# Kernel optimization log

Measured on AMD Instinct MI355X. Metric: run time of the kernel, lower is better.

The kernel has to match this reference:

```python
import jax, jax.numpy as jnp
import numpy as np

B, H, CI, O = 8, 16, 16, 16          # batch, child spatial, child caps, parent caps
K, S, ROUTINGS = 3, 1, 3             # kernel, stride, EM iterations
FINAL_LAMBDA = 0.01
EPS = 1e-9


def setup_inputs() -> dict:
    key = jax.random.key(0)
    k1, k2, k3, k4, k5 = jax.random.split(key, 5)
    inputs_pose = jax.random.normal(k1, (B, H, H, CI, 16), dtype=jnp.float32)
    inputs_activation = jax.random.uniform(k2, (B, H, H, CI, 1), dtype=jnp.float32)
    # transformation matrices: [1, k*k*child_caps, parent_caps, 4, 4]
    w = jax.random.normal(k3, (1, K * K * CI, O, 4, 4), dtype=jnp.float32)
    beta_a = jax.random.normal(k4, (O,), dtype=jnp.float32)
    beta_v = jax.random.normal(k5, (O,), dtype=jnp.float32)
    return {"inputs_pose": inputs_pose, "inputs_activation": inputs_activation,
            "w": w, "beta_a": beta_a, "beta_v": beta_v}


def _extract_patches(x, k, s):
    # kernel_tile: im2col-like gather. x: [B, H, W, ...] -> [B, p, p, k, k, ...]
    Hs = x.shape[1]
    p = (Hs - k) // s + 1
    idx = (jnp.arange(p) * s)[:, None] + jnp.arange(k)[None, :]      # [p, k]
    xh = x[:, idx]                   # [B, ph, kh, W, ...]
    patches = xh[:, :, :, idx]       # [B, ph, kh, pw, kw, ...]
    return jnp.swapaxes(patches, 2, 3), p


def _child_index_map(Hs, k, s, p):
    # flat child spatial index feeding each (parent pos, kernel slot)
    ph = np.arange(p)[:, None] * s + np.arange(k)[None, :]           # [p, k]
    ch = ph[:, None, :, None] * Hs + ph[None, :, None, :]            # [p, p, k, k]
    return ch.reshape(p * p, k * k)                                   # [P2, K2]


def reference(inputs_pose, inputs_activation, w, beta_a, beta_v):
    P = (H - K) // S + 1
    P2, K2 = P * P, K * K
    K2CI = K2 * CI

    # ---- kernel_tile ----
    pose_t, _ = _extract_patches(inputs_pose, K, S)       # [B,P,P,K,K,CI,16]
    act_t, _ = _extract_patches(inputs_activation, K, S)  # [B,P,P,K,K,CI,1]
    pose_unroll = pose_t.reshape(B * P2, K2CI, 4, 4)
    act_unroll = act_t.reshape(B * P2, K2CI)

    # ---- compute_votes: tiny 4x4 matmuls per (child slot, parent cap) ----
    votes = jnp.einsum('nkpq,koqr->nkopr', pose_unroll, w[0])  # [B*P2,K2CI,O,4,4]
    votes = votes.reshape(B, P2, K2CI, O, 16)
    act_i = act_unroll.reshape(B, P2, K2CI, 1, 1)

    # ---- spatial routing bookkeeping (static integers) ----
    child_idx = _child_index_map(H, K, S, P)                    # [P2, K2]
    kk_child = np.repeat(child_idx, CI, axis=1)                 # [P2, K2CI]
    counts = np.zeros(H * H, np.float32)
    np.add.at(counts, child_idx.reshape(-1), 1.0)               # parents per child pos
    cap_id = np.tile(np.arange(CI), K2)                         # [K2CI]
    seg = jnp.asarray((kk_child * CI + cap_id[None, :]).reshape(-1))  # [P2*K2CI]
    n_seg = H * H * CI

    # initial routing: uniform over all (parent pos, parent cap) each child feeds
    rr0 = 1.0 / (O * counts[kk_child])                          # [P2, K2CI]
    rr = jnp.asarray(rr0)[None, :, :, None, None]               # bcast [1,P2,K2CI,1,1]

    beta_a_b = beta_a.reshape(1, 1, 1, O, 1)
    beta_v_b = beta_v.reshape(1, 1, 1, O, 1)

    mean = act_j = None
    for it in range(ROUTINGS):
        inv_temp = FINAL_LAMBDA * (1.0 - 0.95 ** (it + 1))
        # ---- M-step: weighted Gaussian statistics ----
        rr_prime = rr * act_i                                   # [B,P2,K2CI,O,1]
        rr_sum = jnp.sum(rr_prime, axis=2, keepdims=True) + EPS # [B,P2,1,O,1]
        mean = jnp.sum(rr_prime * votes, axis=2, keepdims=True) / rr_sum
        var = jnp.sum(rr_prime * jnp.square(votes - mean), axis=2, keepdims=True) / rr_sum + EPS
        cost_h = (beta_v_b + 0.5 * jnp.log(var)) * rr_sum       # [B,P2,1,O,16]
        cost = jnp.sum(cost_h, axis=-1, keepdims=True)          # [B,P2,1,O,1]
        act_j = jax.nn.sigmoid(inv_temp * (beta_a_b - cost))    # [B,P2,1,O,1]
        # ---- E-step: softmax over all (parent pos, parent cap) per child capsule ----
        if it < ROUTINGS - 1:
            log_p = -0.5 * jnp.sum(jnp.square(votes - mean) / var
                                   + jnp.log(2.0 * np.pi * var), axis=-1)  # [B,P2,K2CI,O]
            zz = jnp.log(act_j[..., 0] + EPS) + log_p           # [B,P2,K2CI,O]
            z = jnp.transpose(zz, (1, 2, 0, 3)).reshape(P2 * K2CI, B, O)
            row_max = jnp.max(z, axis=-1)                       # [P2*K2CI, B]
            seg_max = jax.ops.segment_max(row_max, seg, num_segments=n_seg)
            g = seg_max[seg][..., None]
            ez = jnp.exp(z - g)
            denom = jax.ops.segment_sum(jnp.sum(ez, axis=-1), seg, num_segments=n_seg)[seg]
            rr_new = ez / (denom[..., None] + EPS)              # sums to 1 per child capsule
            rr = jnp.transpose(rr_new.reshape(P2, K2CI, B, O), (2, 0, 1, 3))[..., None]

    pose_out = mean[:, :, 0].reshape(B, P, P, O, 16)
    act_out = act_j[:, :, 0].reshape(B, P, P, O, 1)
    return pose_out, act_out
```

## Files before the change

### kernel.cpp

```cpp
#include <hip/hip_runtime.h>

namespace {
constexpr int B_ = 8, H_ = 16, CI_ = 16, O_ = 16, P_ = 14;
constexpr int P2_ = P_ * P_;
constexpr int K2CI_ = 144;
constexpr int NV_ = 2304;
constexpr float EPS_ = 1e-9f;
constexpr float LOG2PI_ = 1.8378770664093453f;

using f2 = __attribute__((ext_vector_type(2))) float;

__device__ __forceinline__ float cnt1(int h) {
  int lo = (h - (P_ - 1)) > 0 ? (h - (P_ - 1)) : 0;
  int hi = h < 2 ? h : 2;
  return (float)(hi - lo + 1);
}

__global__ __launch_bounds__(256) void transpose_all(const float* __restrict__ pose,
                                                     float* __restrict__ pose_t,
                                                     const float* __restrict__ w,
                                                     float* __restrict__ wt) {
  if (blockIdx.x < 2048) {
    const int i = blockIdx.x * 256 + threadIdx.x;
    const int cell = i >> 4, idx = i & 15;
    const int p = idx >> 2, q = idx & 3;
    pose_t[(cell << 4) + (q << 2) + p] = pose[i];
  } else {
    const int i = (blockIdx.x - 2048) * 256 + threadIdx.x;
    const int ko = i >> 4, q = (i >> 2) & 3, r = i & 3;
    wt[(ko << 4) + (r << 2) + q] = w[i];
  }
}

template <int MODE>
__global__ __launch_bounds__(512, 8) void caps_main(
    const float* __restrict__ pose_t, const float* __restrict__ act,
    const float* __restrict__ wt, const float* __restrict__ beta_a,
    const float* __restrict__ beta_v, const float* __restrict__ zin,
    const float* __restrict__ gmax, const float* __restrict__ gden,
    float* __restrict__ zout, float* __restrict__ out) {
  __shared__ float rr_s[(MODE == 0) ? K2CI_ : NV_];
  __shared__ f2 partv[4][512];
  __shared__ float partr[512];
  __shared__ f2 sfin[4][64];
  __shared__ float sfr[64];
  __shared__ float gm_s[(MODE == 0) ? 1 : K2CI_];
  __shared__ float ad_s[(MODE == 0) ? 1 : K2CI_];

  const int tid = threadIdx.x;
  const int wv = __builtin_amdgcn_readfirstlane(tid >> 6);
  const int l = tid & 63;
  const int o = l >> 2, r = l & 3;
  const int pid = blockIdx.x;
  const int b = pid / P2_;
  const int p2 = pid - b * P2_;
  const int pi = p2 / P_;
  const int pj = p2 - pi * P_;
  const float inv_temp = (MODE == 0) ? 0.0005f : (MODE == 1) ? 0.000975f : 0.00142625f;

  if (MODE == 0) {
    if (tid < K2CI_) {
      const int ci = tid & 15, kk = tid >> 4;
      const int ki = (kk >= 6) ? 2 : (kk >= 3) ? 1 : 0, kj = kk - 3 * ki;
      const int cidx = ((b * H_ + pi + ki) * H_ + pj + kj) * CI_ + ci;
      rr_s[tid] = act[cidx] / (16.0f * cnt1(pi + ki) * cnt1(pj + kj));
    }
  } else {
    if (tid < K2CI_) {
      const int ci = tid & 15, kk = tid >> 4;
      const int ki = (kk >= 6) ? 2 : (kk >= 3) ? 1 : 0, kj = kk - 3 * ki;
      const int cidx = ((b * H_ + pi + ki) * H_ + pj + kj) * CI_ + ci;
      gm_s[tid] = gmax[cidx];
      ad_s[tid] = act[cidx] / (gden[cidx] + EPS_);
    }
    __syncthreads();
    for (int i4 = tid; i4 < NV_ / 4; i4 += 512) {
      const float4 z4 = ((const float4*)(zin + (size_t)pid * NV_))[i4];
      const int k = i4 >> 2;
      const float gmk = gm_s[k], adk = ad_s[k];
      float4 r4;
      r4.x = __expf(z4.x - gmk) * adk;
      r4.y = __expf(z4.y - gmk) * adk;
      r4.z = __expf(z4.z - gmk) * adk;
      r4.w = __expf(z4.w - gmk) * adk;
      ((float4*)rr_s)[i4] = r4;
    }
  }
  __syncthreads();

  const float bvo = 16.0f * beta_v[o];
  const float bao = beta_a[o];

  const float* pose_b = pose_t + ((size_t)((b * H_ + pi) * H_ + pj) << 8);
  const float* wt_l = wt + (l << 2);
  const int ci0 = wv * 2;

#define WT_OFF(idx) ((((idx) >> 1) << 12) + ((ci0 + ((idx)&1)) << 8))
#define PB_OFF(idx) (((((idx) >> 1) / 3) << 12) + ((((idx) >> 1) % 3) << 8) + ((ci0 + ((idx)&1)) << 4))

  float prr = 0.f;
  f2 pm01 = {0.f, 0.f}, pm23 = {0.f, 0.f}, pv01 = {0.f, 0.f}, pv23 = {0.f, 0.f};
  {
    float4 wbuf0 = *(const float4*)(wt_l + WT_OFF(0));
    float4 wbuf1 = *(const float4*)(wt_l + WT_OFF(1));
#pragma unroll
    for (int idx = 0; idx < 18; ++idx) {
      const float4 w4 = (idx & 1) ? wbuf1 : wbuf0;
      if (idx < 16) {
        if (idx & 1)
          wbuf1 = *(const float4*)(wt_l + WT_OFF(idx + 2));
        else
          wbuf0 = *(const float4*)(wt_l + WT_OFF(idx + 2));
      }
      const float* pb = pose_b + PB_OFF(idx);
      const float4 P0 = *(const float4*)(pb);
      const float4 P1 = *(const float4*)(pb + 4);
      const float4 P2 = *(const float4*)(pb + 8);
      const float4 P3 = *(const float4*)(pb + 12);
      f2 v01 = (f2){P0.x, P0.y} * w4.x;
      f2 v23 = (f2){P0.z, P0.w} * w4.x;
      v01 = __builtin_elementwise_fma((f2){P1.x, P1.y}, (f2){w4.y, w4.y}, v01);
      v23 = __builtin_elementwise_fma((f2){P1.z, P1.w}, (f2){w4.y, w4.y}, v23);
      v01 = __builtin_elementwise_fma((f2){P2.x, P2.y}, (f2){w4.z, w4.z}, v01);
      v23 = __builtin_elementwise_fma((f2){P2.z, P2.w}, (f2){w4.z, w4.z}, v23);
      v01 = __builtin_elementwise_fma((f2){P3.x, P3.y}, (f2){w4.w, w4.w}, v01);
      v23 = __builtin_elementwise_fma((f2){P3.z, P3.w}, (f2){w4.w, w4.w}, v23);
      const int k = ((idx >> 1) << 4) + ci0 + (idx & 1);
      const float rrk = (MODE == 0) ? rr_s[k] : rr_s[(k << 4) + o];
      prr += rrk;
      const f2 rr2 = {rrk, rrk};
      const f2 a01 = rr2 * v01, a23 = rr2 * v23;
      pm01 += a01;
      pm23 += a23;
      pv01 = __builtin_elementwise_fma(a01, v01, pv01);
      pv23 = __builtin_elementwise_fma(a23, v23, pv23);
    }
  }
  partv[0][tid] = pm01; partv[1][tid] = pm23;
  partv[2][tid] = pv01; partv[3][tid] = pv23;
  partr[tid] = prr;
  __syncthreads();
  if (tid < 320) {
    if (tid < 256) {
      const int st = tid >> 6, li = tid & 63;
      f2 acc = partv[st][li];
#pragma unroll
      for (int wvi = 1; wvi < 8; ++wvi) acc += partv[st][wvi * 64 + li];
      sfin[st][li] = acc;
    } else {
      const int li = tid & 63;
      float acc = partr[li];
#pragma unroll
      for (int wvi = 1; wvi < 8; ++wvi) acc += partr[wvi * 64 + li];
      sfr[li] = acc;
    }
  }
  __syncthreads();
  const f2 S01 = sfin[0][l], S23 = sfin[1][l];
  const f2 V01 = sfin[2][l], V23 = sfin[3][l];
  const float rsum = sfr[l] + EPS_;
  const float irs = 1.0f / rsum;
  const f2 irs2 = {irs, irs};
  const f2 m01 = S01 * irs2, m23 = S23 * irs2;
  const f2 zero2 = {0.f, 0.f}, eps2 = {EPS_, EPS_};
  const f2 va01 = __builtin_elementwise_max(V01 * irs2 - m01 * m01, zero2) + eps2;
  const f2 va23 = __builtin_elementwise_max(V23 * irs2 - m23 * m23, zero2) + eps2;
  float slv = __logf(va01.x) + __logf(va01.y) + __logf(va23.x) + __logf(va23.y);
  slv += __shfl_xor(slv, 1);
  slv += __shfl_xor(slv, 2);
  const float cost = (bvo + 0.5f * slv) * rsum;
  const float aj = 1.0f / (1.0f + __expf(-inv_temp * (bao - cost)));

  if (MODE == 2) {
    if (wv == 0) {
      float* ob = out + ((size_t)(pid * 16 + o) << 4) + r;
      ob[0] = m01.x; ob[4] = m01.y; ob[8] = m23.x; ob[12] = m23.y;
      if (r == 0) out[(size_t)B_ * P2_ * O_ * 16 + pid * 16 + o] = aj;
    }
    return;
  }

  const f2 iv01 = {1.0f / va01.x, 1.0f / va01.y};
  const f2 iv23 = {1.0f / va23.x, 1.0f / va23.y};
  const float Cz = __logf(aj + EPS_) - 0.5f * (slv + 16.0f * LOG2PI_);
  float* zo = zout + (size_t)pid * NV_ + o;
  {
    float4 wbuf0 = *(const float4*)(wt_l + WT_OFF(0));
    float4 wbuf1 = *(const float4*)(wt_l + WT_OFF(1));
#pragma unroll
    for (int idx = 0; idx < 18; ++idx) {
      const float4 w4 = (idx & 1) ? wbuf1 : wbuf0;
      if (idx < 16) {
        if (idx & 1)
          wbuf1 = *(const float4*)(wt_l + WT_OFF(idx + 2));
        else
          wbuf0 = *(const float4*)(wt_l + WT_OFF(idx + 2));
      }
      const float* pb = pose_b + PB_OFF(idx);
      const float4 P0 = *(const float4*)(pb);
      const float4 P1 = *(const float4*)(pb + 4);
      const float4 P2 = *(const float4*)(pb + 8);
      const float4 P3 = *(const float4*)(pb + 12);
      f2 v01 = (f2){P0.x, P0.y} * w4.x;
      f2 v23 = (f2){P0.z, P0.w} * w4.x;
      v01 = __builtin_elementwise_fma((f2){P1.x, P1.y}, (f2){w4.y, w4.y}, v01);
      v23 = __builtin_elementwise_fma((f2){P1.z, P1.w}, (f2){w4.y, w4.y}, v23);
      v01 = __builtin_elementwise_fma((f2){P2.x, P2.y}, (f2){w4.z, w4.z}, v01);
      v23 = __builtin_elementwise_fma((f2){P2.z, P2.w}, (f2){w4.z, w4.z}, v23);
      v01 = __builtin_elementwise_fma((f2){P3.x, P3.y}, (f2){w4.w, w4.w}, v01);
      v23 = __builtin_elementwise_fma((f2){P3.z, P3.w}, (f2){w4.w, w4.w}, v23);
      const f2 d01 = v01 - m01, d23 = v23 - m23;
      const f2 q2 = __builtin_elementwise_fma(d01 * d01, iv01, (d23 * d23) * iv23);
      float q = q2.x + q2.y;
      q += __shfl_xor(q, 1);
      q += __shfl_xor(q, 2);
      const int k = ((idx >> 1) << 4) + ci0 + (idx & 1);
      if (r == 0) zo[k << 4] = Cz - 0.5f * q;
    }
  }
#undef WT_OFF
#undef PB_OFF
}

__global__ __launch_bounds__(256) void seg_reduce(const float* __restrict__ z,
                                                  float* __restrict__ gmax,
                                                  float* __restrict__ gden) {
  const int tid = blockIdx.x * 256 + threadIdx.x;
  const int part = tid & 3, ci = (tid >> 2) & 15, w2 = (tid >> 6) & 15;
  const int h = (tid >> 10) & 15, b = tid >> 14;
  float4 v[9];
  float m = -3.0e38f;
#pragma unroll
  for (int s = 0; s < 9; ++s) {
    const int ki = (s >= 6) ? 2 : (s >= 3) ? 1 : 0, kj = s - 3 * ki;
    const int pi = h - ki, pj = w2 - kj;
    if ((unsigned)pi < (unsigned)P_ && (unsigned)pj < (unsigned)P_) {
      v[s] = *(const float4*)(z + (size_t)(b * P2_ + pi * P_ + pj) * NV_ + s * 256 +
                              ci * 16 + part * 4);
    } else {
      v[s] = make_float4(-3.0e38f, -3.0e38f, -3.0e38f, -3.0e38f);
    }
    m = fmaxf(m, fmaxf(fmaxf(v[s].x, v[s].y), fmaxf(v[s].z, v[s].w)));
  }
  m = fmaxf(m, __shfl_xor(m, 1));
  m = fmaxf(m, __shfl_xor(m, 2));
  float s_ = 0.f;
#pragma unroll
  for (int s = 0; s < 9; ++s) {
    s_ += __expf(v[s].x - m) + __expf(v[s].y - m) + __expf(v[s].z - m) + __expf(v[s].w - m);
  }
  s_ += __shfl_xor(s_, 1);
  s_ += __shfl_xor(s_, 2);
  if (part == 0) {
    gmax[tid >> 2] = m;
    gden[tid >> 2] = s_;
  }
}
}

extern "C" void kernel_launch(void* const* d_in, const int* in_sizes, int n_in,
                              void* d_out, int out_size, void* d_ws, size_t ws_size,
                              hipStream_t stream) {
  const float* pose = (const float*)d_in[0];
  const float* act = (const float*)d_in[1];
  const float* w = (const float*)d_in[2];
  const float* ba = (const float*)d_in[3];
  const float* bv = (const float*)d_in[4];
  float* out = (float*)d_out;

  float* z = (float*)d_ws;
  float* gm = z + (size_t)B_ * P2_ * NV_;
  float* gd = gm + B_ * H_ * H_ * CI_;
  float* wt = gd + B_ * H_ * H_ * CI_;
  float* pt = wt + 36864;

  const int NB = B_ * P2_;
  transpose_all<<<2192, 256, 0, stream>>>(pose, pt, w, wt);
  caps_main<0><<<NB, 512, 0, stream>>>(pt, act, wt, ba, bv, z, gm, gd, z, out);
  seg_reduce<<<512, 256, 0, stream>>>(z, gm, gd);
  caps_main<1><<<NB, 512, 0, stream>>>(pt, act, wt, ba, bv, z, gm, gd, z, out);
  seg_reduce<<<512, 256, 0, stream>>>(z, gm, gd);
  caps_main<2><<<NB, 512, 0, stream>>>(pt, act, wt, ba, bv, z, gm, gd, z, out);
}
```

Before: 164.0 us.

## Fuse pose transpose into caps_main via shared-memory staging of patch poses

```diff
diff --git a/kernel.cpp b/kernel.cpp
--- a/kernel.cpp
+++ b/kernel.cpp
@@ -16,29 +16,21 @@
   return (float)(hi - lo + 1);
 }
 
-__global__ __launch_bounds__(256) void transpose_all(const float* __restrict__ pose,
-                                                     float* __restrict__ pose_t,
-                                                     const float* __restrict__ w,
-                                                     float* __restrict__ wt) {
-  if (blockIdx.x < 2048) {
-    const int i = blockIdx.x * 256 + threadIdx.x;
-    const int cell = i >> 4, idx = i & 15;
-    const int p = idx >> 2, q = idx & 3;
-    pose_t[(cell << 4) + (q << 2) + p] = pose[i];
-  } else {
-    const int i = (blockIdx.x - 2048) * 256 + threadIdx.x;
-    const int ko = i >> 4, q = (i >> 2) & 3, r = i & 3;
-    wt[(ko << 4) + (r << 2) + q] = w[i];
-  }
+__global__ __launch_bounds__(256) void transpose_w(const float* __restrict__ w,
+                                                   float* __restrict__ wt) {
+  const int i = blockIdx.x * 256 + threadIdx.x;
+  const int ko = i >> 4, q = (i >> 2) & 3, r = i & 3;
+  wt[(ko << 4) + (r << 2) + q] = w[i];
 }
 
 template <int MODE>
 __global__ __launch_bounds__(512, 8) void caps_main(
-    const float* __restrict__ pose_t, const float* __restrict__ act,
+    const float* __restrict__ pose, const float* __restrict__ act,
     const float* __restrict__ wt, const float* __restrict__ beta_a,
     const float* __restrict__ beta_v, const float* __restrict__ zin,
     const float* __restrict__ gmax, const float* __restrict__ gden,
     float* __restrict__ zout, float* __restrict__ out) {
+  __shared__ __align__(16) float pose_s[NV_];
   __shared__ float rr_s[(MODE == 0) ? K2CI_ : NV_];
   __shared__ f2 partv[4][512];
   __shared__ float partr[512];
@@ -58,21 +50,29 @@
   const int pj = p2 - pi * P_;
   const float inv_temp = (MODE == 0) ? 0.0005f : (MODE == 1) ? 0.000975f : 0.00142625f;
 
-  if (MODE == 0) {
-    if (tid < K2CI_) {
-      const int ci = tid & 15, kk = tid >> 4;
-      const int ki = (kk >= 6) ? 2 : (kk >= 3) ? 1 : 0, kj = kk - 3 * ki;
-      const int cidx = ((b * H_ + pi + ki) * H_ + pj + kj) * CI_ + ci;
+  if (tid < K2CI_) {
+    const int ci = tid & 15, kk = tid >> 4;
+    const int ki = (kk >= 6) ? 2 : (kk >= 3) ? 1 : 0, kj = kk - 3 * ki;
+    const float* src = pose + ((size_t)((b * H_ + pi + ki) * H_ + pj + kj) << 8) + (ci << 4);
+    const float4 R0 = *(const float4*)(src);
+    const float4 R1 = *(const float4*)(src + 4);
+    const float4 R2 = *(const float4*)(src + 8);
+    const float4 R3 = *(const float4*)(src + 12);
+    float4* dst = (float4*)(pose_s + (kk << 8) + (ci << 4));
+    dst[0] = make_float4(R0.x, R1.x, R2.x, R3.x);
+    dst[1] = make_float4(R0.y, R1.y, R2.y, R3.y);
+    dst[2] = make_float4(R0.z, R1.z, R2.z, R3.z);
+    dst[3] = make_float4(R0.w, R1.w, R2.w, R3.w);
+
+    const int cidx = ((b * H_ + pi + ki) * H_ + pj + kj) * CI_ + ci;
+    if (MODE == 0) {
       rr_s[tid] = act[cidx] / (16.0f * cnt1(pi + ki) * cnt1(pj + kj));
-    }
-  } else {
-    if (tid < K2CI_) {
-      const int ci = tid & 15, kk = tid >> 4;
-      const int ki = (kk >= 6) ? 2 : (kk >= 3) ? 1 : 0, kj = kk - 3 * ki;
-      const int cidx = ((b * H_ + pi + ki) * H_ + pj + kj) * CI_ + ci;
+    } else {
       gm_s[tid] = gmax[cidx];
       ad_s[tid] = act[cidx] / (gden[cidx] + EPS_);
     }
+  }
+  if (MODE != 0) {
     __syncthreads();
     for (int i4 = tid; i4 < NV_ / 4; i4 += 512) {
       const float4 z4 = ((const float4*)(zin + (size_t)pid * NV_))[i4];
@@ -91,12 +91,11 @@
   const float bvo = 16.0f * beta_v[o];
   const float bao = beta_a[o];
 
-  const float* pose_b = pose_t + ((size_t)((b * H_ + pi) * H_ + pj) << 8);
   const float* wt_l = wt + (l << 2);
   const int ci0 = wv * 2;
 
 #define WT_OFF(idx) ((((idx) >> 1) << 12) + ((ci0 + ((idx)&1)) << 8))
-#define PB_OFF(idx) (((((idx) >> 1) / 3) << 12) + ((((idx) >> 1) % 3) << 8) + ((ci0 + ((idx)&1)) << 4))
+#define PB_OFF(idx) ((((idx) >> 1) << 8) + ((ci0 + ((idx)&1)) << 4))
 
   float prr = 0.f;
   f2 pm01 = {0.f, 0.f}, pm23 = {0.f, 0.f}, pv01 = {0.f, 0.f}, pv23 = {0.f, 0.f};
@@ -112,7 +111,7 @@
         else
           wbuf0 = *(const float4*)(wt_l + WT_OFF(idx + 2));
       }
-      const float* pb = pose_b + PB_OFF(idx);
+      const float* pb = pose_s + PB_OFF(idx);
       const float4 P0 = *(const float4*)(pb);
       const float4 P1 = *(const float4*)(pb + 4);
       const float4 P2 = *(const float4*)(pb + 8);
@@ -196,7 +195,7 @@
         else
           wbuf0 = *(const float4*)(wt_l + WT_OFF(idx + 2));
       }
-      const float* pb = pose_b + PB_OFF(idx);
+      const float* pb = pose_s + PB_OFF(idx);
       const float4 P0 = *(const float4*)(pb);
       const float4 P1 = *(const float4*)(pb + 4);
       const float4 P2 = *(const float4*)(pb + 8);
@@ -272,13 +271,12 @@
   float* gm = z + (size_t)B_ * P2_ * NV_;
   float* gd = gm + B_ * H_ * H_ * CI_;
   float* wt = gd + B_ * H_ * H_ * CI_;
-  float* pt = wt + 36864;
 
   const int NB = B_ * P2_;
-  transpose_all<<<2192, 256, 0, stream>>>(pose, pt, w, wt);
-  caps_main<0><<<NB, 512, 0, stream>>>(pt, act, wt, ba, bv, z, gm, gd, z, out);
+  transpose_w<<<144, 256, 0, stream>>>(w, wt);
+  caps_main<0><<<NB, 512, 0, stream>>>(pose, act, wt, ba, bv, z, gm, gd, z, out);
   seg_reduce<<<512, 256, 0, stream>>>(z, gm, gd);
-  caps_main<1><<<NB, 512, 0, stream>>>(pt, act, wt, ba, bv, z, gm, gd, z, out);
+  caps_main<1><<<NB, 512, 0, stream>>>(pose, act, wt, ba, bv, z, gm, gd, z, out);
   seg_reduce<<<512, 256, 0, stream>>>(z, gm, gd);
-  caps_main<2><<<NB, 512, 0, stream>>>(pt, act, wt, ba, bv, z, gm, gd, z, out);
-}
+  caps_main<2><<<NB, 512, 0, stream>>>(pose, act, wt, ba, bv, z, gm, gd, z, out);
+}
```

Result: slower. 170.3 us (+3.9%).

## Fuse segment softmax reduction into routing kernel and cache votes in registers

Applied to the files above, without the earlier changes.

```diff
diff --git a/kernel.cpp b/kernel.cpp
--- a/kernel.cpp
+++ b/kernel.cpp
@@ -3,6 +3,7 @@
 namespace {
 constexpr int B_ = 8, H_ = 16, CI_ = 16, O_ = 16, P_ = 14;
 constexpr int P2_ = P_ * P_;
+constexpr int NB_ = B_ * P2_;
 constexpr int K2CI_ = 144;
 constexpr int NV_ = 2304;
 constexpr float EPS_ = 1e-9f;
@@ -33,11 +34,10 @@
 }
 
 template <int MODE>
-__global__ __launch_bounds__(512, 8) void caps_main(
+__global__ __launch_bounds__(512, 4) void caps_main(
     const float* __restrict__ pose_t, const float* __restrict__ act,
     const float* __restrict__ wt, const float* __restrict__ beta_a,
     const float* __restrict__ beta_v, const float* __restrict__ zin,
-    const float* __restrict__ gmax, const float* __restrict__ gden,
     float* __restrict__ zout, float* __restrict__ out) {
   __shared__ float rr_s[(MODE == 0) ? K2CI_ : NV_];
   __shared__ f2 partv[4][512];
@@ -46,6 +46,8 @@
   __shared__ float sfr[64];
   __shared__ float gm_s[(MODE == 0) ? 1 : K2CI_];
   __shared__ float ad_s[(MODE == 0) ? 1 : K2CI_];
+  __shared__ float pmax_s[(MODE == 0) ? 1 : K2CI_][3];
+  __shared__ float psum_s[(MODE == 0) ? 1 : K2CI_][3];
 
   const int tid = threadIdx.x;
   const int wv = __builtin_amdgcn_readfirstlane(tid >> 6);
@@ -66,12 +68,52 @@
       rr_s[tid] = act[cidx] / (16.0f * cnt1(pi + ki) * cnt1(pj + kj));
     }
   } else {
+    const int child = tid / 3;
+    const int s3 = tid - child * 3;
+    float4 vz[12];
+    if (tid < 432) {
+      const int cci = child & 15, kk = child >> 4;
+      const int ki = (kk >= 6) ? 2 : (kk >= 3) ? 1 : 0, kj = kk - 3 * ki;
+      const int hh = pi + ki, ww = pj + kj;
+      float pm = -3.0e38f;
+#pragma unroll
+      for (int j = 0; j < 3; ++j) {
+        const int cs = s3 * 3 + j;
+        const int ki2 = (cs >= 6) ? 2 : (cs >= 3) ? 1 : 0, kj2 = cs - 3 * ki2;
+        const int pi2 = hh - ki2, pj2 = ww - kj2;
+        const bool ok = (unsigned)pi2 < (unsigned)P_ && (unsigned)pj2 < (unsigned)P_;
+        const float* zp = zin + (size_t)(b * P2_ + pi2 * P_ + pj2) * NV_ +
+                          (cs << 8) + (cci << 4);
+#pragma unroll
+        for (int q4 = 0; q4 < 4; ++q4) {
+          vz[j * 4 + q4] = ok ? *(const float4*)(zp + q4 * 4)
+                              : make_float4(-3.0e38f, -3.0e38f, -3.0e38f, -3.0e38f);
+          const float4 t4 = vz[j * 4 + q4];
+          pm = fmaxf(pm, fmaxf(fmaxf(t4.x, t4.y), fmaxf(t4.z, t4.w)));
+        }
+      }
+      pmax_s[child][s3] = pm;
+    }
+    __syncthreads();
+    if (tid < K2CI_)
+      gm_s[tid] = fmaxf(fmaxf(pmax_s[tid][0], pmax_s[tid][1]), pmax_s[tid][2]);
+    __syncthreads();
+    if (tid < 432) {
+      const float g = gm_s[child];
+      float ps = 0.f;
+#pragma unroll
+      for (int i = 0; i < 12; ++i) {
+        ps += __expf(vz[i].x - g) + __expf(vz[i].y - g) + __expf(vz[i].z - g) +
+              __expf(vz[i].w - g);
+      }
+      psum_s[child][s3] = ps;
+    }
+    __syncthreads();
     if (tid < K2CI_) {
-      const int ci = tid & 15, kk = tid >> 4;
+      const int cci = tid & 15, kk = tid >> 4;
       const int ki = (kk >= 6) ? 2 : (kk >= 3) ? 1 : 0, kj = kk - 3 * ki;
-      const int cidx = ((b * H_ + pi + ki) * H_ + pj + kj) * CI_ + ci;
-      gm_s[tid] = gmax[cidx];
-      ad_s[tid] = act[cidx] / (gden[cidx] + EPS_);
+      const int cidx = ((b * H_ + pi + ki) * H_ + pj + kj) * CI_ + cci;
+      ad_s[tid] = act[cidx] / (psum_s[tid][0] + psum_s[tid][1] + psum_s[tid][2] + EPS_);
     }
     __syncthreads();
     for (int i4 = tid; i4 < NV_ / 4; i4 += 512) {
@@ -98,6 +140,7 @@
 #define WT_OFF(idx) ((((idx) >> 1) << 12) + ((ci0 + ((idx)&1)) << 8))
 #define PB_OFF(idx) (((((idx) >> 1) / 3) << 12) + ((((idx) >> 1) % 3) << 8) + ((ci0 + ((idx)&1)) << 4))
 
+  f2 vc01[18], vc23[18];
   float prr = 0.f;
   f2 pm01 = {0.f, 0.f}, pm23 = {0.f, 0.f}, pv01 = {0.f, 0.f}, pv23 = {0.f, 0.f};
   {
@@ -125,6 +168,10 @@
       v23 = __builtin_elementwise_fma((f2){P2.z, P2.w}, (f2){w4.z, w4.z}, v23);
       v01 = __builtin_elementwise_fma((f2){P3.x, P3.y}, (f2){w4.w, w4.w}, v01);
       v23 = __builtin_elementwise_fma((f2){P3.z, P3.w}, (f2){w4.w, w4.w}, v23);
+      if (MODE != 2) {
+        vc01[idx] = v01;
+        vc23[idx] = v23;
+      }
       const int k = ((idx >> 1) << 4) + ci0 + (idx & 1);
       const float rrk = (MODE == 0) ? rr_s[k] : rr_s[(k << 4) + o];
       prr += rrk;
@@ -185,31 +232,9 @@
   const float Cz = __logf(aj + EPS_) - 0.5f * (slv + 16.0f * LOG2PI_);
   float* zo = zout + (size_t)pid * NV_ + o;
   {
-    float4 wbuf0 = *(const float4*)(wt_l + WT_OFF(0));
-    float4 wbuf1 = *(const float4*)(wt_l + WT_OFF(1));
 #pragma unroll
     for (int idx = 0; idx < 18; ++idx) {
-      const float4 w4 = (idx & 1) ? wbuf1 : wbuf0;
-      if (idx < 16) {
-        if (idx & 1)
-          wbuf1 = *(const float4*)(wt_l + WT_OFF(idx + 2));
-        else
-          wbuf0 = *(const float4*)(wt_l + WT_OFF(idx + 2));
-      }
-      const float* pb = pose_b + PB_OFF(idx);
-      const float4 P0 = *(const float4*)(pb);
-      const float4 P1 = *(const float4*)(pb + 4);
-      const float4 P2 = *(const float4*)(pb + 8);
-      const float4 P3 = *(const float4*)(pb + 12);
-      f2 v01 = (f2){P0.x, P0.y} * w4.x;
-      f2 v23 = (f2){P0.z, P0.w} * w4.x;
-      v01 = __builtin_elementwise_fma((f2){P1.x, P1.y}, (f2){w4.y, w4.y}, v01);
-      v23 = __builtin_elementwise_fma((f2){P1.z, P1.w}, (f2){w4.y, w4.y}, v23);
-      v01 = __builtin_elementwise_fma((f2){P2.x, P2.y}, (f2){w4.z, w4.z}, v01);
-      v23 = __builtin_elementwise_fma((f2){P2.z, P2.w}, (f2){w4.z, w4.z}, v23);
-      v01 = __builtin_elementwise_fma((f2){P3.x, P3.y}, (f2){w4.w, w4.w}, v01);
-      v23 = __builtin_elementwise_fma((f2){P3.z, P3.w}, (f2){w4.w, w4.w}, v23);
-      const f2 d01 = v01 - m01, d23 = v23 - m23;
+      const f2 d01 = vc01[idx] - m01, d23 = vc23[idx] - m23;
       const f2 q2 = __builtin_elementwise_fma(d01 * d01, iv01, (d23 * d23) * iv23);
       float q = q2.x + q2.y;
       q += __shfl_xor(q, 1);
@@ -220,41 +245,6 @@
   }
 #undef WT_OFF
 #undef PB_OFF
-}
-
-__global__ __launch_bounds__(256) void seg_reduce(const float* __restrict__ z,
-                                                  float* __restrict__ gmax,
-                                                  float* __restrict__ gden) {
-  const int tid = blockIdx.x * 256 + threadIdx.x;
-  const int part = tid & 3, ci = (tid >> 2) & 15, w2 = (tid >> 6) & 15;
-  const int h = (tid >> 10) & 15, b = tid >> 14;
-  float4 v[9];
-  float m = -3.0e38f;
-#pragma unroll
-  for (int s = 0; s < 9; ++s) {
-    const int ki = (s >= 6) ? 2 : (s >= 3) ? 1 : 0, kj = s - 3 * ki;
-    const int pi = h - ki, pj = w2 - kj;
-    if ((unsigned)pi < (unsigned)P_ && (unsigned)pj < (unsigned)P_) {
-      v[s] = *(const float4*)(z + (size_t)(b * P2_ + pi * P_ + pj) * NV_ + s * 256 +
-                              ci * 16 + part * 4);
-    } else {
-      v[s] = make_float4(-3.0e38f, -3.0e38f, -3.0e38f, -3.0e38f);
-    }
-    m = fmaxf(m, fmaxf(fmaxf(v[s].x, v[s].y), fmaxf(v[s].z, v[s].w)));
-  }
-  m = fmaxf(m, __shfl_xor(m, 1));
-  m = fmaxf(m, __shfl_xor(m, 2));
-  float s_ = 0.f;
-#pragma unroll
-  for (int s = 0; s < 9; ++s) {
-    s_ += __expf(v[s].x - m) + __expf(v[s].y - m) + __expf(v[s].z - m) + __expf(v[s].w - m);
-  }
-  s_ += __shfl_xor(s_, 1);
-  s_ += __shfl_xor(s_, 2);
-  if (part == 0) {
-    gmax[tid >> 2] = m;
-    gden[tid >> 2] = s_;
-  }
 }
 }
 
@@ -268,17 +258,13 @@
   const float* bv = (const float*)d_in[4];
   float* out = (float*)d_out;
 
-  float* z = (float*)d_ws;
-  float* gm = z + (size_t)B_ * P2_ * NV_;
-  float* gd = gm + B_ * H_ * H_ * CI_;
-  float* wt = gd + B_ * H_ * H_ * CI_;
+  float* z0 = (float*)d_ws;
+  float* z1 = z0 + (size_t)NB_ * NV_;
+  float* wt = z1 + (size_t)NB_ * NV_;
   float* pt = wt + 36864;
 
-  const int NB = B_ * P2_;
   transpose_all<<<2192, 256, 0, stream>>>(pose, pt, w, wt);
-  caps_main<0><<<NB, 512, 0, stream>>>(pt, act, wt, ba, bv, z, gm, gd, z, out);
-  seg_reduce<<<512, 256, 0, stream>>>(z, gm, gd);
-  caps_main<1><<<NB, 512, 0, stream>>>(pt, act, wt, ba, bv, z, gm, gd, z, out);
-  seg_reduce<<<512, 256, 0, stream>>>(z, gm, gd);
-  caps_main<2><<<NB, 512, 0, stream>>>(pt, act, wt, ba, bv, z, gm, gd, z, out);
-}
+  caps_main<0><<<NB_, 512, 0, stream>>>(pt, act, wt, ba, bv, nullptr, z0, out);
+  caps_main<1><<<NB_, 512, 0, stream>>>(pt, act, wt, ba, bv, z0, z1, out);
+  caps_main<2><<<NB_, 512, 0, stream>>>(pt, act, wt, ba, bv, z1, nullptr, out);
+}
```

New measurement: 181.0 us. 1.1x slower.
